# Kernel optimization log

Hardware: AMD Instinct MI355X
Metric: run time of the kernel (lower is better)

Reference implementation:

```python
import jax, jax.numpy as jnp
import numpy as np

B, CIN, COUT, H, W = 8, 128, 128, 64, 64
KH = KW = 3
STRIDE = PAD = 1
DIL = 1
K = KH * KW
EPS = 1e-4


def setup_inputs() -> dict:
    key = jax.random.key(0)
    k1, k2, k3 = jax.random.split(key, 3)
    Ho = (H + 2 * PAD - DIL * (KH - 1) - 1) // STRIDE + 1
    Wo = (W + 2 * PAD - DIL * (KW - 1) - 1) // STRIDE + 1
    x = jax.random.normal(k1, (B, CIN, H, W), dtype=jnp.float32)
    offset = jax.random.normal(k2, (B, 2 * K, Ho, Wo), dtype=jnp.float32)
    weight = jax.random.normal(k3, (COUT, CIN, KH, KW), dtype=jnp.float32) * 0.05
    return {"x": x, "offset": offset, "weight": weight}


def _bilinear_gather(x, py, px):
    # x: [B, C, H, W]; py/px: [B, K, Ho, Wo] float sampling positions
    Bn, C, Hn, Wn = x.shape
    x_flat = x.reshape(Bn, C, Hn * Wn)
    y0 = jnp.floor(py)
    x0 = jnp.floor(px)
    ly = py - y0  # fractional parts
    lx = px - x0
    out = 0.0
    corners = [(0.0, 0.0, (1 - ly) * (1 - lx)), (0.0, 1.0, (1 - ly) * lx),
               (1.0, 0.0, ly * (1 - lx)), (1.0, 1.0, ly * lx)]
    for dy, dx, wgt in corners:
        yy = y0 + dy
        xx = x0 + dx
        valid = (yy >= 0) & (yy < Hn) & (xx >= 0) & (xx < Wn)
        yi = jnp.clip(yy, 0, Hn - 1).astype(jnp.int32)
        xi = jnp.clip(xx, 0, Wn - 1).astype(jnp.int32)
        idx = (yi * Wn + xi).reshape(Bn, -1)  # [B, K*Ho*Wo]
        g = jax.vmap(lambda xf, ib: jnp.take(xf, ib, axis=1))(x_flat, idx)  # [B, C, N]
        out = out + g * (wgt * valid.astype(x.dtype)).reshape(Bn, 1, -1)
    return out  # [B, C, K*Ho*Wo]


def reference(x, offset, weight) -> jnp.ndarray:
    Bn = x.shape[0]
    Ho, Wo = offset.shape[2], offset.shape[3]
    # --- weight normalization (per output channel, per kernel tap) ---
    norm_fac = (KH * KW) ** 0.5
    length = jnp.sqrt(jnp.sum(jnp.square(weight) + EPS, axis=1, keepdims=True))  # [O,1,kh,kw]
    wn = weight / length / norm_fac  # [O, Cin, kh, kw]
    # --- sampling positions ---
    off = offset.reshape(Bn, K, 2, Ho, Wo)
    off_y, off_x = off[:, :, 0], off[:, :, 1]
    ky, kx = jnp.meshgrid(jnp.arange(KH), jnp.arange(KW), indexing="ij")
    ky = (ky.reshape(K) * DIL).astype(jnp.float32)
    kx = (kx.reshape(K) * DIL).astype(jnp.float32)
    base_y = (jnp.arange(Ho) * STRIDE - PAD).astype(jnp.float32)
    base_x = (jnp.arange(Wo) * STRIDE - PAD).astype(jnp.float32)
    py = base_y[None, None, :, None] + ky[None, :, None, None] + off_y  # [B,K,Ho,Wo]
    px = base_x[None, None, None, :] + kx[None, :, None, None] + off_x
    # --- deformable im2col + GEMM ---
    cols = _bilinear_gather(x, py, px).reshape(Bn, CIN, K, Ho, Wo)
    out = jnp.einsum("bckhw,ock->bohw", cols, wn.reshape(COUT, CIN, K))
    return out
```

## Files before the change

kernel.cpp:

```cpp
#include <hip/hip_runtime.h>
#include <hip/hip_bf16.h>
#include <hip/hip_fp16.h>
#include <math.h>


typedef __attribute__((ext_vector_type(8))) short short8;
typedef __attribute__((ext_vector_type(4))) float floatx4;

static __device__ __forceinline__ unsigned int f2bf(float f) {
    unsigned int u = __float_as_uint(f);
    u += 0x7fffu + ((u >> 16) & 1u);
    return u >> 16;
}
static __device__ __forceinline__ float bflo(unsigned int w) {
    return __uint_as_float(w << 16);
}
static __device__ __forceinline__ float bfhi(unsigned int w) {
    return __uint_as_float(w & 0xffff0000u);
}
static __device__ __forceinline__ unsigned int packbf2(float lo, float hi) {
    __hip_bfloat162 h = __float22bfloat162_rn(make_float2(lo, hi));
    unsigned int u;
    __builtin_memcpy(&u, &h, 4);
    return u;
}

__global__ void prep_k(const float* __restrict__ x, const float* __restrict__ w,
                       unsigned int* __restrict__ xt32, unsigned short* __restrict__ wb) {
    __shared__ float lds[128 * 65];
    const int tid = threadIdx.x;

    if (blockIdx.x < 512) {
        const int b = blockIdx.x & 7, h = (blockIdx.x >> 3) & 63;
        const float* xp = x + (b * 128 * 64 + h) * 64;
        #pragma unroll 4
        for (int i = 0; i < 32; i++) {
            const int c = i * 4 + (tid >> 6);
            const int ww = tid & 63;
            lds[c * 65 + ww] = xp[c * 4096 + ww];
        }
        __syncthreads();
        unsigned int* xo = xt32 + (b * 64 + h) * 4096;
        #pragma unroll 4
        for (int i = 0; i < 16; i++) {
            const int flat2 = i * 256 + tid;
            const int ww = flat2 >> 6, cp = flat2 & 63;
            xo[flat2] = packbf2(lds[(2 * cp) * 65 + ww], lds[(2 * cp + 1) * 65 + ww]);
        }
    } else {
        const int o = (blockIdx.x - 512) * 4 + (tid >> 6);
        const int lane = tid & 63;
        const float* wo = w + o * 1152;
        float v[18];
        #pragma unroll
        for (int i = 0; i < 18; i++) v[i] = wo[lane * 18 + i];
        float s[9];
        #pragma unroll
        for (int k = 0; k < 9; k++) s[k] = v[k] * v[k] + v[9 + k] * v[9 + k];
        #pragma unroll
        for (int d = 32; d >= 1; d >>= 1) {
            #pragma unroll
            for (int k = 0; k < 9; k++) s[k] += __shfl_xor(s[k], d, 64);
        }
        const int c0 = 2 * lane, c1 = c0 + 1;
        #pragma unroll
        for (int k = 0; k < 9; k++) {
            const float inv = 1.0f / (3.0f * sqrtf(s[k] + 0.0128f));
            wb[((k * 16 + (c0 >> 3)) * 128 + o) * 8 + (c0 & 7)] = (unsigned short)f2bf(v[k] * inv);
            wb[((k * 16 + (c1 >> 3)) * 128 + o) * 8 + (c1 & 7)] = (unsigned short)f2bf(v[9 + k] * inv);
        }
    }
}

static __device__ __forceinline__ unsigned int bl1(const float w0, const float w1,
                                                   const float w2, const float w3,
                                                   unsigned int r0, unsigned int r1,
                                                   unsigned int r2, unsigned int r3) {
    const float lo = w0*bflo(r0) + w1*bflo(r1) + w2*bflo(r2) + w3*bflo(r3);
    const float hi = w0*bfhi(r0) + w1*bfhi(r1) + w2*bfhi(r2) + w3*bfhi(r3);
    return packbf2(lo, hi);
}

static __device__ __forceinline__ uint4 combine4(const float4 wvv,
                                                 const uint4 r0, const uint4 r1,
                                                 const uint4 r2, const uint4 r3) {
    uint4 pk;
    pk.x = bl1(wvv.x, wvv.y, wvv.z, wvv.w, r0.x, r1.x, r2.x, r3.x);
    pk.y = bl1(wvv.x, wvv.y, wvv.z, wvv.w, r0.y, r1.y, r2.y, r3.y);
    pk.z = bl1(wvv.x, wvv.y, wvv.z, wvv.w, r0.z, r1.z, r2.z, r3.z);
    pk.w = bl1(wvv.x, wvv.y, wvv.z, wvv.w, r0.w, r1.w, r2.w, r3.w);
    return pk;
}

__global__ __launch_bounds__(256, 4) void dconv_k(
    const unsigned short* __restrict__ xt, const float* __restrict__ off,
    const unsigned short* __restrict__ wb, float* __restrict__ out)
{
    __shared__ float4 tapw[288];
    __shared__ int4   tapi[288];
    __shared__ alignas(16) unsigned short colsS[2][16 * 264];

    const int idx = blockIdx.x;
    const int b = idx & 7;
    const int ho = (idx >> 3) & 63;
    const int pix0 = (idx >> 9) * 32;
    const int tid = threadIdx.x;

    for (int t = tid; t < 288; t += 256) {
        const int k = t >> 5, p = t & 31;
        const int pw = pix0 + p;
        const int oidx = ((b * 18 + 2 * k) * 64 + ho) * 64 + pw;
        const float offy = off[oidx];
        const float offx = off[oidx + 4096];
        const float py = (float)(ho - 1 + (k / 3)) + offy;
        const float px = (float)(pw - 1 + (k % 3)) + offx;
        const float y0f = floorf(py), x0f = floorf(px);
        const float ly = py - y0f, lx = px - x0f;
        const int y0 = (int)y0f, x0 = (int)x0f;
        const int y1 = y0 + 1, x1 = x0 + 1;
        const float vy0 = (y0 >= 0 && y0 < 64) ? 1.0f : 0.0f;
        const float vy1 = (y1 >= 0 && y1 < 64) ? 1.0f : 0.0f;
        const float vx0 = (x0 >= 0 && x0 < 64) ? 1.0f : 0.0f;
        const float vx1 = (x1 >= 0 && x1 < 64) ? 1.0f : 0.0f;
        const int yc0 = min(max(y0, 0), 63), yc1 = min(max(y1, 0), 63);
        const int xc0 = min(max(x0, 0), 63), xc1 = min(max(x1, 0), 63);
        tapw[t] = make_float4((1.0f - ly) * (1.0f - lx) * vy0 * vx0,
                              (1.0f - ly) * lx          * vy0 * vx1,
                              ly * (1.0f - lx)          * vy1 * vx0,
                              ly * lx                   * vy1 * vx1);
        tapi[t] = make_int4((yc0 * 64 + xc0) * 128, (yc0 * 64 + xc1) * 128,
                            (yc1 * 64 + xc0) * 128, (yc1 * 64 + xc1) * 128);
    }
    __syncthreads();

    const int lane = tid & 63, wv = tid >> 6;
    const int quad = lane >> 4, l16 = lane & 15;
    const int g = tid & 15, prow = tid >> 4;
    const unsigned short* xb = xt + b * (64 * 64 * 128);
    const int wbase = wv * 32;

    floatx4 acc0[2], acc1[2];
    #pragma unroll
    for (int t = 0; t < 2; t++) { acc0[t] = (floatx4)0.0f; acc1[t] = (floatx4)0.0f; }

    #pragma unroll
    for (int i = 0; i < 2; i++) {
        const int p = i * 16 + prow;
        const float4 wvv = tapw[p];
        const int4  iv  = tapi[p];
        const uint4 r0 = *(const uint4*)(xb + iv.x + g * 8);
        const uint4 r1 = *(const uint4*)(xb + iv.y + g * 8);
        const uint4 r2 = *(const uint4*)(xb + iv.z + g * 8);
        const uint4 r3 = *(const uint4*)(xb + iv.w + g * 8);
        *(uint4*)&colsS[0][g * 264 + p * 8] = combine4(wvv, r0, r1, r2, r3);
    }
    __syncthreads();

    for (int k = 0; k < 9; k++) {
        const int cur = k & 1;

        const unsigned short* wk = wb + k * 16384;
        short8 a0[4], a1[4];
        #pragma unroll
        for (int q = 0; q < 4; q++) {
            const int cgrp = q * 4 + quad;
            a0[q] = *(const short8*)(wk + (cgrp * 128 + wbase + l16) * 8);
            a1[q] = *(const short8*)(wk + (cgrp * 128 + wbase + 16 + l16) * 8);
        }

        uint4 r[2][4];
        if (k < 8) {
            #pragma unroll
            for (int i = 0; i < 2; i++) {
                const int p = i * 16 + prow;
                const int4 iv = tapi[(k + 1) * 32 + p];
                r[i][0] = *(const uint4*)(xb + iv.x + g * 8);
                r[i][1] = *(const uint4*)(xb + iv.y + g * 8);
                r[i][2] = *(const uint4*)(xb + iv.z + g * 8);
                r[i][3] = *(const uint4*)(xb + iv.w + g * 8);
            }
        }

        #pragma unroll
        for (int q = 0; q < 4; q++) {
            const int cgrp = q * 4 + quad;
            #pragma unroll
            for (int t = 0; t < 2; t++) {
                const short8 bf = *(const short8*)&colsS[cur][cgrp * 264 + (t * 16 + l16) * 8];
                acc0[t] = __builtin_amdgcn_mfma_f32_16x16x32_bf16(a0[q], bf, acc0[t], 0, 0, 0);
                acc1[t] = __builtin_amdgcn_mfma_f32_16x16x32_bf16(a1[q], bf, acc1[t], 0, 0, 0);
            }
        }

        if (k < 8) {
            #pragma unroll
            for (int i = 0; i < 2; i++) {
                const int p = i * 16 + prow;
                const float4 wvv = tapw[(k + 1) * 32 + p];
                *(uint4*)&colsS[cur ^ 1][g * 264 + p * 8] =
                    combine4(wvv, r[i][0], r[i][1], r[i][2], r[i][3]);
            }
            __syncthreads();
        }
    }

    float* ob = out + b * 128 * 4096 + ho * 64 + pix0;
    #pragma unroll
    for (int t = 0; t < 2; t++) {
        const int pix = t * 16 + l16;
        #pragma unroll
        for (int r2 = 0; r2 < 4; r2++) {
            __builtin_nontemporal_store(acc0[t][r2], &ob[(wbase + quad * 4 + r2) * 4096 + pix]);
            __builtin_nontemporal_store(acc1[t][r2], &ob[(wbase + 16 + quad * 4 + r2) * 4096 + pix]);
        }
    }
}

extern "C" void kernel_launch(void* const* d_in, const int* in_sizes, int n_in,
                              void* d_out, int out_size, void* d_ws, size_t ws_size,
                              hipStream_t stream) {
    const float* x   = (const float*)d_in[0];
    const float* off = (const float*)d_in[1];
    const float* w   = (const float*)d_in[2];
    float* out = (float*)d_out;

    unsigned short* xt = (unsigned short*)d_ws;
    unsigned short* wbuf = xt + 8 * 64 * 64 * 128;

    hipLaunchKernelGGL(prep_k,  dim3(544),  dim3(256), 0, stream,
                       x, w, (unsigned int*)xt, wbuf);
    hipLaunchKernelGGL(dconv_k, dim3(1024), dim3(256), 0, stream, xt, off, wbuf, out);
}
```

Baseline: 99.27 us.

## Process full output row per block with 512 threads and compact tap encoding

Each block now covers a whole 64-pixel output row with 8 waves of 16 output channels each, instead of 32 pixels with 4 waves of 32 channels. Grid size halves and threads per block double. Per-tap sampling data is stored in shared memory as a packed 8-byte record (fp16 fractions plus 8-bit base coordinates) and expanded into weights and indices on use, which saves shared memory at the cost of extra ALU work. Weight A-fragments are now reused across four pixel tiles instead of two, and fp16 rounding of the fractional parts adds a small precision risk.

Result: no change. 99.01 us, median of 2 (-0.3%).

```diff
diff --git a/kernel.cpp b/kernel.cpp
--- a/kernel.cpp
+++ b/kernel.cpp
@@ -92,67 +92,72 @@
     return pk;
 }
 
-__global__ __launch_bounds__(256, 4) void dconv_k(
+static __device__ __forceinline__ void tap_expand(const uint2 tp, float4& wvv, int4& iv) {
+    const float ly = __half2float(__ushort_as_half((unsigned short)(tp.x & 0xffff)));
+    const float lx = __half2float(__ushort_as_half((unsigned short)(tp.x >> 16)));
+    const int y0 = (int)(tp.y & 0xFF) - 32;
+    const int x0 = (int)((tp.y >> 8) & 0xFF) - 32;
+    const int y1 = y0 + 1, x1 = x0 + 1;
+    const float fy0 = (y0 >= 0 && y0 < 64) ? (1.0f - ly) : 0.0f;
+    const float fy1 = (y1 >= 0 && y1 < 64) ? ly : 0.0f;
+    const float fx0 = (x0 >= 0 && x0 < 64) ? (1.0f - lx) : 0.0f;
+    const float fx1 = (x1 >= 0 && x1 < 64) ? lx : 0.0f;
+    const int yc0 = min(max(y0, 0), 63), yc1 = min(max(y1, 0), 63);
+    const int xc0 = min(max(x0, 0), 63), xc1 = min(max(x1, 0), 63);
+    wvv = make_float4(fy0 * fx0, fy0 * fx1, fy1 * fx0, fy1 * fx1);
+    iv = make_int4((yc0 * 64 + xc0) << 7, (yc0 * 64 + xc1) << 7,
+                   (yc1 * 64 + xc0) << 7, (yc1 * 64 + xc1) << 7);
+}
+
+__global__ __launch_bounds__(512, 4) void dconv_k(
     const unsigned short* __restrict__ xt, const float* __restrict__ off,
     const unsigned short* __restrict__ wb, float* __restrict__ out)
 {
-    __shared__ float4 tapw[288];
-    __shared__ int4   tapi[288];
-    __shared__ alignas(16) unsigned short colsS[2][16 * 264];
+    __shared__ uint2 tapP[576];
+    __shared__ alignas(16) unsigned short colsS[2][16 * 520];
 
     const int idx = blockIdx.x;
     const int b = idx & 7;
     const int ho = (idx >> 3) & 63;
-    const int pix0 = (idx >> 9) * 32;
     const int tid = threadIdx.x;
 
-    for (int t = tid; t < 288; t += 256) {
-        const int k = t >> 5, p = t & 31;
-        const int pw = pix0 + p;
-        const int oidx = ((b * 18 + 2 * k) * 64 + ho) * 64 + pw;
+    for (int t = tid; t < 576; t += 512) {
+        const int k = t >> 6, p = t & 63;
+        const int oidx = ((b * 18 + 2 * k) * 64 + ho) * 64 + p;
         const float offy = off[oidx];
         const float offx = off[oidx + 4096];
         const float py = (float)(ho - 1 + (k / 3)) + offy;
-        const float px = (float)(pw - 1 + (k % 3)) + offx;
+        const float px = (float)(p - 1 + (k % 3)) + offx;
         const float y0f = floorf(py), x0f = floorf(px);
-        const float ly = py - y0f, lx = px - x0f;
-        const int y0 = (int)y0f, x0 = (int)x0f;
-        const int y1 = y0 + 1, x1 = x0 + 1;
-        const float vy0 = (y0 >= 0 && y0 < 64) ? 1.0f : 0.0f;
-        const float vy1 = (y1 >= 0 && y1 < 64) ? 1.0f : 0.0f;
-        const float vx0 = (x0 >= 0 && x0 < 64) ? 1.0f : 0.0f;
-        const float vx1 = (x1 >= 0 && x1 < 64) ? 1.0f : 0.0f;
-        const int yc0 = min(max(y0, 0), 63), yc1 = min(max(y1, 0), 63);
-        const int xc0 = min(max(x0, 0), 63), xc1 = min(max(x1, 0), 63);
-        tapw[t] = make_float4((1.0f - ly) * (1.0f - lx) * vy0 * vx0,
-                              (1.0f - ly) * lx          * vy0 * vx1,
-                              ly * (1.0f - lx)          * vy1 * vx0,
-                              ly * lx                   * vy1 * vx1);
-        tapi[t] = make_int4((yc0 * 64 + xc0) * 128, (yc0 * 64 + xc1) * 128,
-                            (yc1 * 64 + xc0) * 128, (yc1 * 64 + xc1) * 128);
+        uint2 pk;
+        pk.x = (unsigned int)__half_as_ushort(__float2half_rn(py - y0f)) |
+               ((unsigned int)__half_as_ushort(__float2half_rn(px - x0f)) << 16);
+        pk.y = (unsigned int)(((int)y0f + 32) & 0xFF) |
+               ((unsigned int)(((int)x0f + 32) & 0xFF) << 8);
+        tapP[t] = pk;
     }
     __syncthreads();
 
     const int lane = tid & 63, wv = tid >> 6;
     const int quad = lane >> 4, l16 = lane & 15;
-    const int g = tid & 15, prow = tid >> 4;
+    const int g = tid & 15, p0 = tid >> 4;
     const unsigned short* xb = xt + b * (64 * 64 * 128);
-    const int wbase = wv * 32;
-
-    floatx4 acc0[2], acc1[2];
+    const int obase = wv * 16;
+
+    floatx4 acc[4];
     #pragma unroll
-    for (int t = 0; t < 2; t++) { acc0[t] = (floatx4)0.0f; acc1[t] = (floatx4)0.0f; }
+    for (int t = 0; t < 4; t++) acc[t] = (floatx4)0.0f;
 
     #pragma unroll
     for (int i = 0; i < 2; i++) {
-        const int p = i * 16 + prow;
-        const float4 wvv = tapw[p];
-        const int4  iv  = tapi[p];
+        const int p = p0 + i * 32;
+        float4 wvv; int4 iv;
+        tap_expand(tapP[p], wvv, iv);
         const uint4 r0 = *(const uint4*)(xb + iv.x + g * 8);
         const uint4 r1 = *(const uint4*)(xb + iv.y + g * 8);
         const uint4 r2 = *(const uint4*)(xb + iv.z + g * 8);
         const uint4 r3 = *(const uint4*)(xb + iv.w + g * 8);
-        *(uint4*)&colsS[0][g * 264 + p * 8] = combine4(wvv, r0, r1, r2, r3);
+        *(uint4*)&colsS[0][g * 520 + p * 8] = combine4(wvv, r0, r1, r2, r3);
     }
     __syncthreads();
 
@@ -160,24 +165,24 @@
         const int cur = k & 1;
 
         const unsigned short* wk = wb + k * 16384;
-        short8 a0[4], a1[4];
+        short8 a[4];
         #pragma unroll
         for (int q = 0; q < 4; q++) {
             const int cgrp = q * 4 + quad;
-            a0[q] = *(const short8*)(wk + (cgrp * 128 + wbase + l16) * 8);
-            a1[q] = *(const short8*)(wk + (cgrp * 128 + wbase + 16 + l16) * 8);
+            a[q] = *(const short8*)(wk + (cgrp * 128 + obase + l16) * 8);
         }
 
         uint4 r[2][4];
+        float4 wvv[2]; int4 ivd[2];
         if (k < 8) {
             #pragma unroll
             for (int i = 0; i < 2; i++) {
-                const int p = i * 16 + prow;
-                const int4 iv = tapi[(k + 1) * 32 + p];
-                r[i][0] = *(const uint4*)(xb + iv.x + g * 8);
-                r[i][1] = *(const uint4*)(xb + iv.y + g * 8);
-                r[i][2] = *(const uint4*)(xb + iv.z + g * 8);
-                r[i][3] = *(const uint4*)(xb + iv.w + g * 8);
+                const int p = p0 + i * 32;
+                tap_expand(tapP[(k + 1) * 64 + p], wvv[i], ivd[i]);
+                r[i][0] = *(const uint4*)(xb + ivd[i].x + g * 8);
+                r[i][1] = *(const uint4*)(xb + ivd[i].y + g * 8);
+                r[i][2] = *(const uint4*)(xb + ivd[i].z + g * 8);
+                r[i][3] = *(const uint4*)(xb + ivd[i].w + g * 8);
             }
         }
 
@@ -185,33 +190,31 @@
         for (int q = 0; q < 4; q++) {
             const int cgrp = q * 4 + quad;
             #pragma unroll
-            for (int t = 0; t < 2; t++) {
-                const short8 bf = *(const short8*)&colsS[cur][cgrp * 264 + (t * 16 + l16) * 8];
-                acc0[t] = __builtin_amdgcn_mfma_f32_16x16x32_bf16(a0[q], bf, acc0[t], 0, 0, 0);
-                acc1[t] = __builtin_amdgcn_mfma_f32_16x16x32_bf16(a1[q], bf, acc1[t], 0, 0, 0);
+            for (int t = 0; t < 4; t++) {
+                const short8 bf = *(const short8*)&colsS[cur][cgrp * 520 + (t * 16 + l16) * 8];
+                acc[t] = __builtin_amdgcn_mfma_f32_16x16x32_bf16(a[q], bf, acc[t], 0, 0, 0);
             }
         }
 
         if (k < 8) {
             #pragma unroll
             for (int i = 0; i < 2; i++) {
-                const int p = i * 16 + prow;
-                const float4 wvv = tapw[(k + 1) * 32 + p];
-                *(uint4*)&colsS[cur ^ 1][g * 264 + p * 8] =
-                    combine4(wvv, r[i][0], r[i][1], r[i][2], r[i][3]);
+                const int p = p0 + i * 32;
+                *(uint4*)&colsS[cur ^ 1][g * 520 + p * 8] =
+                    combine4(wvv[i], r[i][0], r[i][1], r[i][2], r[i][3]);
             }
             __syncthreads();
         }
     }
 
-    float* ob = out + b * 128 * 4096 + ho * 64 + pix0;
+    float* ob = out + b * 128 * 4096 + ho * 64;
     #pragma unroll
-    for (int t = 0; t < 2; t++) {
+    for (int t = 0; t < 4; t++) {
         const int pix = t * 16 + l16;
         #pragma unroll
         for (int r2 = 0; r2 < 4; r2++) {
-            __builtin_nontemporal_store(acc0[t][r2], &ob[(wbase + quad * 4 + r2) * 4096 + pix]);
-            __builtin_nontemporal_store(acc1[t][r2], &ob[(wbase + 16 + quad * 4 + r2) * 4096 + pix]);
+            __builtin_nontemporal_store(acc[t][r2],
+                &ob[(obase + quad * 4 + r2) * 4096 + pix]);
         }
     }
 }
@@ -227,7 +230,7 @@
     unsigned short* xt = (unsigned short*)d_ws;
     unsigned short* wbuf = xt + 8 * 64 * 64 * 128;
 
-    hipLaunchKernelGGL(prep_k,  dim3(544),  dim3(256), 0, stream,
+    hipLaunchKernelGGL(prep_k,  dim3(544), dim3(256), 0, stream,
                        x, w, (unsigned int*)xt, wbuf);
-    hipLaunchKernelGGL(dconv_k, dim3(1024), dim3(256), 0, stream, xt, off, wbuf, out);
-}
+    hipLaunchKernelGGL(dconv_k, dim3(512), dim3(512), 0, stream, xt, off, wbuf, out);
+}
```
